# Kernel tuning notes

Measured on AMD Instinct MI355X. Metric: run time of the kernel, lower is better.

The kernel has to match this reference:

```python
import jax, jax.numpy as jnp
import numpy as np

DIM = 128
N_HEADS = 4
HEAD_DIM = DIM // N_HEADS
K = 16
B, N = 2, 8192
BIAS_HID = 32


def knn_idx(xyz, k):
    # squared pairwise distances: [B,N,N] (same argsort order as cdist)
    sq = jnp.sum(xyz * xyz, axis=-1)  # [B,N]
    d2 = sq[:, :, None] + sq[:, None, :] - 2.0 * jnp.einsum('bnd,bmd->bnm', xyz, xyz)
    _, idx = jax.lax.top_k(-d2, k)  # smallest distances
    return idx  # [B,N,k]


def setup_inputs() -> dict:
    key = jax.random.key(0)
    ks = jax.random.split(key, 12)
    s = 1.0 / np.sqrt(DIM)
    inp = {
        'x':   jax.random.normal(ks[0], (B, N, DIM), jnp.float32),
        'xyz': jax.random.normal(ks[1], (B, N, 3), jnp.float32),
        'Wq': jax.random.uniform(ks[2], (DIM, DIM), jnp.float32, -s, s),
        'bq': jnp.zeros((DIM,), jnp.float32),
        'Wk': jax.random.uniform(ks[3], (DIM, DIM), jnp.float32, -s, s),
        'bk': jnp.zeros((DIM,), jnp.float32),
        'Wv': jax.random.uniform(ks[4], (DIM, DIM), jnp.float32, -s, s),
        'bv': jnp.zeros((DIM,), jnp.float32),
        'Wo': jax.random.uniform(ks[5], (DIM, DIM), jnp.float32, -s, s),
        'bo': jnp.zeros((DIM,), jnp.float32),
        'W1': jax.random.uniform(ks[6], (3, BIAS_HID), jnp.float32, -0.5, 0.5),
        'b1': jnp.zeros((BIAS_HID,), jnp.float32),
        'W2': jax.random.uniform(ks[7], (BIAS_HID, N_HEADS), jnp.float32, -1.0 / np.sqrt(BIAS_HID), 1.0 / np.sqrt(BIAS_HID)),
        'b2': jnp.zeros((N_HEADS,), jnp.float32),
    }
    return inp


def reference(x, xyz, Wq, bq, Wk, bk, Wv, bv, Wo, bo, W1, b1, W2, b2):
    Bb, Nn, C = x.shape
    idx = knn_idx(xyz, K)  # [B,N,k]

    q = (x @ Wq + bq).reshape(Bb, Nn, N_HEADS, HEAD_DIM)
    kf = (x @ Wk + bk).reshape(Bb, Nn, N_HEADS, HEAD_DIM)
    vf = (x @ Wv + bv).reshape(Bb, Nn, N_HEADS, HEAD_DIM)

    gather = jax.vmap(lambda f, i: f[i])  # per-batch fancy gather
    kn = gather(kf, idx)  # [B,N,k,H,D]
    vn = gather(vf, idx)  # [B,N,k,H,D]
    nxyz = gather(xyz, idx)  # [B,N,k,3]

    rel = xyz[:, :, None, :] - nxyz  # [B,N,k,3]
    bias = jax.nn.relu(rel @ W1 + b1) @ W2 + b2  # [B,N,k,H]

    scores = jnp.einsum('bnhd,bnkhd->bnhk', q, kn) / np.sqrt(HEAD_DIM)
    scores = scores + jnp.swapaxes(bias, 2, 3)  # [B,N,H,k]
    attn = jax.nn.softmax(scores, axis=-1)
    out = jnp.einsum('bnhk,bnkhd->bnhd', attn, vn).reshape(Bb, Nn, C)
    return out @ Wo + bo
```

## Files before the change

kernel.cpp:

```cpp
#include <hip/hip_runtime.h>
#include <hip/hip_bf16.h>
#include <math.h>

#define BATCH 2
#define NPT   8192
#define DIMC  128
#define NH    4
#define KNN_K 16
#define HID   32
#define BN    (BATCH*NPT)

#define TILE 1024
#define QPW  2
#define NWV  4

__device__ __forceinline__ float readlane_f(float v, int l) {
  return __int_as_float(__builtin_amdgcn_readlane(__float_as_int(v), l));
}

__global__ __launch_bounds__(256) void knn_kernel(const float* __restrict__ xyz,
                                                  int* __restrict__ knn_out) {
  __shared__ float4 spts[TILE];
  const int tid  = threadIdx.x;
  const int lane = tid & 63;
  const int wave = tid >> 6;
  const int qbase = blockIdx.x * (NWV*QPW) + wave * QPW;
  const int b = qbase / NPT;

  float qx[QPW], qy[QPW], qz[QPW], qsq[QPW];
  float topd[QPW]; int topi[QPW]; float tau[QPW];
#pragma unroll
  for (int qi = 0; qi < QPW; ++qi) {
    const int g = qbase + qi;
    qx[qi] = xyz[(size_t)g*3+0];
    qy[qi] = xyz[(size_t)g*3+1];
    qz[qi] = xyz[(size_t)g*3+2];
    qsq[qi] = __fadd_rn(__fadd_rn(__fmul_rn(qx[qi],qx[qi]),
                                  __fmul_rn(qy[qi],qy[qi])),
                        __fmul_rn(qz[qi],qz[qi]));
    topd[qi] = 3e38f; topi[qi] = 0; tau[qi] = 3e38f;
  }

  for (int t = 0; t < NPT/TILE; ++t) {
    __syncthreads();
    const float* src = xyz + (size_t)(b*NPT + t*TILE)*3;
    for (int i = tid; i < TILE; i += 256) {
      const float x = src[i*3+0], y = src[i*3+1], z = src[i*3+2];
      const float sq = __fadd_rn(__fadd_rn(__fmul_rn(x,x), __fmul_rn(y,y)),
                                 __fmul_rn(z,z));
      spts[i] = make_float4(x+x, y+y, z+z, sq);
    }
    __syncthreads();

    for (int c = 0; c < TILE/64; ++c) {
      const float4 cd = spts[c*64 + lane];
      const int cbase = t*TILE + c*64;
#pragma unroll
      for (int qi = 0; qi < QPW; ++qi) {
        float dot2 = __fadd_rn(__fadd_rn(__fmul_rn(qx[qi],cd.x),
                                         __fmul_rn(qy[qi],cd.y)),
                               __fmul_rn(qz[qi],cd.z));
        float d2 = __fsub_rn(__fadd_rn(qsq[qi], cd.w), dot2);
        unsigned long long m = __ballot(d2 < tau[qi]);
        while (m) {
          const int l = (int)__builtin_ctzll(m);
          const float dn = readlane_f(d2, l);
          const int   ni_ = cbase + l;
          const float my  = topd[qi];
          const int   myi = topi[qi];
          float ab  = __shfl_up(my, 1);
          int   abi = __shfl_up(myi, 1);
          if (lane == 0) ab = -3e38f;
          const bool ge = dn < my;
          const bool gt = dn < ab;
          topd[qi] = ge ? (gt ? ab  : dn ) : my;
          topi[qi] = ge ? (gt ? abi : ni_) : myi;
          tau[qi] = readlane_f(topd[qi], 15);
          m &= (m - 1);
          if (m) m &= __ballot(d2 < tau[qi]);
        }
      }
    }
  }

#pragma unroll
  for (int qi = 0; qi < QPW; ++qi) {
    if (lane < KNN_K) knn_out[(size_t)(qbase + qi)*KNN_K + lane] = topi[qi];
  }
}

__device__ __forceinline__ float f4c(const float4 v, int u) {
  return u == 0 ? v.x : u == 1 ? v.y : u == 2 ? v.z : v.w;
}

__global__ __launch_bounds__(256) void qkv_kernel(const float* __restrict__ x,
    const float* __restrict__ Wq, const float* __restrict__ bq,
    const float* __restrict__ Wk, const float* __restrict__ bk,
    const float* __restrict__ Wv, const float* __restrict__ bv,
    float* __restrict__ q, float* __restrict__ k, float* __restrict__ v) {
  __shared__ float xs[16*DIMC];
  const int tid = threadIdx.x;
  const int rowbase = blockIdx.x * 16;
  {
    float4* xs4 = (float4*)xs;
    const float4* src4 = (const float4*)(x + (size_t)rowbase*DIMC);
    for (int i = tid; i < 16*DIMC/4; i += 256) xs4[i] = src4[i];
  }
  __syncthreads();

  const int cg = tid & 31, rg = tid >> 5;
  const int c0 = cg * 4;
  float4 aq0 = *(const float4*)&bq[c0], aq1 = aq0;
  float4 ak0 = *(const float4*)&bk[c0], ak1 = ak0;
  float4 av0 = *(const float4*)&bv[c0], av1 = av0;

  for (int kk = 0; kk < DIMC; kk += 4) {
    const float4 xa = *(const float4*)&xs[rg*DIMC + kk];
    const float4 xb = *(const float4*)&xs[(rg+8)*DIMC + kk];
#pragma unroll
    for (int u = 0; u < 4; ++u) {
      const float4 wq = *(const float4*)&Wq[(size_t)(kk+u)*DIMC + c0];
      const float4 wk = *(const float4*)&Wk[(size_t)(kk+u)*DIMC + c0];
      const float4 wv = *(const float4*)&Wv[(size_t)(kk+u)*DIMC + c0];
      const float xau = f4c(xa, u), xbu = f4c(xb, u);
      aq0.x = fmaf(xau, wq.x, aq0.x); aq0.y = fmaf(xau, wq.y, aq0.y);
      aq0.z = fmaf(xau, wq.z, aq0.z); aq0.w = fmaf(xau, wq.w, aq0.w);
      aq1.x = fmaf(xbu, wq.x, aq1.x); aq1.y = fmaf(xbu, wq.y, aq1.y);
      aq1.z = fmaf(xbu, wq.z, aq1.z); aq1.w = fmaf(xbu, wq.w, aq1.w);
      ak0.x = fmaf(xau, wk.x, ak0.x); ak0.y = fmaf(xau, wk.y, ak0.y);
      ak0.z = fmaf(xau, wk.z, ak0.z); ak0.w = fmaf(xau, wk.w, ak0.w);
      ak1.x = fmaf(xbu, wk.x, ak1.x); ak1.y = fmaf(xbu, wk.y, ak1.y);
      ak1.z = fmaf(xbu, wk.z, ak1.z); ak1.w = fmaf(xbu, wk.w, ak1.w);
      av0.x = fmaf(xau, wv.x, av0.x); av0.y = fmaf(xau, wv.y, av0.y);
      av0.z = fmaf(xau, wv.z, av0.z); av0.w = fmaf(xau, wv.w, av0.w);
      av1.x = fmaf(xbu, wv.x, av1.x); av1.y = fmaf(xbu, wv.y, av1.y);
      av1.z = fmaf(xbu, wv.z, av1.z); av1.w = fmaf(xbu, wv.w, av1.w);
    }
  }

  const size_t r0 = (size_t)(rowbase + rg)*DIMC + c0;
  const size_t r1 = (size_t)(rowbase + rg + 8)*DIMC + c0;
  *(float4*)&q[r0] = aq0; *(float4*)&q[r1] = aq1;
  *(float4*)&k[r0] = ak0; *(float4*)&k[r1] = ak1;
  *(float4*)&v[r0] = av0; *(float4*)&v[r1] = av1;
}

__global__ __launch_bounds__(256) void attn_kernel(const float* __restrict__ xyz,
    const int* __restrict__ knn, const float* __restrict__ qb,
    const float* __restrict__ kb, const float* __restrict__ vb,
    const float* __restrict__ W1, const float* __restrict__ b1,
    const float* __restrict__ W2, const float* __restrict__ b2,
    float* __restrict__ ao) {
  __shared__ float sbias[2][NH][KNN_K];
  const int tid = threadIdx.x;
  const int pt  = tid >> 7;
  const int d   = tid & 127;
  const int h   = d >> 5;
  const int p   = blockIdx.x * 2 + pt;
  const int b   = p / NPT;

  int nidx[KNN_K];
#pragma unroll
  for (int j = 0; j < KNN_K; ++j) nidx[j] = knn[(size_t)p*KNN_K + j];

  if (d < 64) {
    const int h2 = d >> 4, j2 = d & 15;
    const float qx0 = xyz[(size_t)p*3+0];
    const float qy0 = xyz[(size_t)p*3+1];
    const float qz0 = xyz[(size_t)p*3+2];
    const size_t nn = (size_t)(b*NPT + nidx[j2]);
    const float rx = qx0 - xyz[nn*3+0];
    const float ry = qy0 - xyz[nn*3+1];
    const float rz = qz0 - xyz[nn*3+2];
    float acc = b2[h2];
#pragma unroll 4
    for (int u = 0; u < HID; ++u) {
      float hv = rx*W1[0*HID+u] + ry*W1[1*HID+u] + rz*W1[2*HID+u] + b1[u];
      hv = hv > 0.f ? hv : 0.f;
      acc = fmaf(hv, W2[u*NH + h2], acc);
    }
    sbias[pt][h2][j2] = acc;
  }

  const float qd = qb[(size_t)p*DIMC + d];
  float s[KNN_K], vr[KNN_K];
#pragma unroll
  for (int j = 0; j < KNN_K; ++j) {
    const size_t row = ((size_t)(b*NPT + nidx[j]))*DIMC + d;
    float t = qd * kb[row];
    vr[j] = vb[row];
    t += __shfl_xor(t, 1, 32);
    t += __shfl_xor(t, 2, 32);
    t += __shfl_xor(t, 4, 32);
    t += __shfl_xor(t, 8, 32);
    t += __shfl_xor(t, 16, 32);
    s[j] = t;
  }
  __syncthreads();

  const float sc = 0.17677669529663689f;
  float mx = -3e38f;
#pragma unroll
  for (int j = 0; j < KNN_K; ++j) {
    s[j] = s[j]*sc + sbias[pt][h][j];
    mx = fmaxf(mx, s[j]);
  }
  float sum = 0.f;
#pragma unroll
  for (int j = 0; j < KNN_K; ++j) { s[j] = expf(s[j]-mx); sum += s[j]; }
  const float inv = 1.f / sum;
  float out = 0.f;
#pragma unroll
  for (int j = 0; j < KNN_K; ++j) out = fmaf(s[j]*inv, vr[j], out);
  ao[(size_t)p*DIMC + d] = out;
}

__global__ __launch_bounds__(256) void proj_kernel(float* __restrict__ inout,
    const float* __restrict__ Wo, const float* __restrict__ bo) {
  __shared__ float xs[16*DIMC];
  const int tid = threadIdx.x;
  const int rowbase = blockIdx.x * 16;
  {
    float4* xs4 = (float4*)xs;
    const float4* src4 = (const float4*)(inout + (size_t)rowbase*DIMC);
    for (int i = tid; i < 16*DIMC/4; i += 256) xs4[i] = src4[i];
  }
  __syncthreads();

  const int cg = tid & 31, rg = tid >> 5;
  const int c0 = cg * 4;
  float4 a0 = *(const float4*)&bo[c0], a1 = a0;

  for (int kk = 0; kk < DIMC; kk += 4) {
    const float4 xa = *(const float4*)&xs[rg*DIMC + kk];
    const float4 xb = *(const float4*)&xs[(rg+8)*DIMC + kk];
#pragma unroll
    for (int u = 0; u < 4; ++u) {
      const float4 w = *(const float4*)&Wo[(size_t)(kk+u)*DIMC + c0];
      const float xau = f4c(xa, u), xbu = f4c(xb, u);
      a0.x = fmaf(xau, w.x, a0.x); a0.y = fmaf(xau, w.y, a0.y);
      a0.z = fmaf(xau, w.z, a0.z); a0.w = fmaf(xau, w.w, a0.w);
      a1.x = fmaf(xbu, w.x, a1.x); a1.y = fmaf(xbu, w.y, a1.y);
      a1.z = fmaf(xbu, w.z, a1.z); a1.w = fmaf(xbu, w.w, a1.w);
    }
  }

  *(float4*)&inout[(size_t)(rowbase + rg)*DIMC + c0]     = a0;
  *(float4*)&inout[(size_t)(rowbase + rg + 8)*DIMC + c0] = a1;
}

extern "C" void kernel_launch(void* const* d_in, const int* in_sizes, int n_in,
                              void* d_out, int out_size, void* d_ws, size_t ws_size,
                              hipStream_t stream) {
  const float* x   = (const float*)d_in[0];
  const float* xyz = (const float*)d_in[1];
  const float* Wq  = (const float*)d_in[2];
  const float* bq  = (const float*)d_in[3];
  const float* Wk  = (const float*)d_in[4];
  const float* bk  = (const float*)d_in[5];
  const float* Wv  = (const float*)d_in[6];
  const float* bv  = (const float*)d_in[7];
  const float* Wo  = (const float*)d_in[8];
  const float* bo  = (const float*)d_in[9];
  const float* W1  = (const float*)d_in[10];
  const float* b1  = (const float*)d_in[11];
  const float* W2  = (const float*)d_in[12];
  const float* b2  = (const float*)d_in[13];
  float* out = (float*)d_out;

  char* ws = (char*)d_ws;
  int*   knn = (int*)ws;
  float* q   = (float*)(ws + (size_t)(1u<<20));
  float* k   = (float*)(ws + (size_t)9*(1u<<20));
  float* v   = (float*)(ws + (size_t)17*(1u<<20));

  hipLaunchKernelGGL(knn_kernel, dim3(BN/(NWV*QPW)), dim3(256), 0, stream, xyz, knn);
  hipLaunchKernelGGL(qkv_kernel, dim3(BN/16), dim3(256), 0, stream,
                     x, Wq, bq, Wk, bk, Wv, bv, q, k, v);
  hipLaunchKernelGGL(attn_kernel, dim3(BN/2), dim3(256), 0, stream,
                     xyz, knn, q, k, v, W1, b1, W2, b2, out);
  hipLaunchKernelGGL(proj_kernel, dim3(BN/16), dim3(256), 0, stream,
                     out, Wo, bo);
}
```

Measured before the change: 203.0 us.

## Remap attention to one wave per point with lane-per-(head,neighbor) scores

The attention kernel now gives each point a single 64-lane wave, with each lane owning one (head, neighbor) pair. Each lane computes its position-bias MLP and a 32-wide q·k dot product with float4 loads. The per-lane shuffle reductions over head dims are replaced by DPP row rotations that reduce max and sum across 16 neighbors. The softmax weights and neighbor indices are staged in shared memory, and each lane then accumulates two output channels from the gathered V rows. This removes redundant bias work and shuffle-heavy reductions and lets each block handle four points. In exchange, K rows are read with a strided per-lane access pattern rather than coalesced across lanes.

```diff
diff --git a/kernel.cpp b/kernel.cpp
--- a/kernel.cpp
+++ b/kernel.cpp
@@ -145,74 +145,92 @@
   *(float4*)&v[r0] = av0; *(float4*)&v[r1] = av1;
 }
 
+template <int CTRL>
+__device__ __forceinline__ float dppf(float x) {
+  return __int_as_float(__builtin_amdgcn_update_dpp(
+      __float_as_int(x), __float_as_int(x), CTRL, 0xF, 0xF, false));
+}
+#define ROR1 0x121
+#define ROR2 0x122
+#define ROR4 0x124
+#define ROR8 0x128
+
 __global__ __launch_bounds__(256) void attn_kernel(const float* __restrict__ xyz,
     const int* __restrict__ knn, const float* __restrict__ qb,
     const float* __restrict__ kb, const float* __restrict__ vb,
     const float* __restrict__ W1, const float* __restrict__ b1,
     const float* __restrict__ W2, const float* __restrict__ b2,
     float* __restrict__ ao) {
-  __shared__ float sbias[2][NH][KNN_K];
-  const int tid = threadIdx.x;
-  const int pt  = tid >> 7;
-  const int d   = tid & 127;
-  const int h   = d >> 5;
-  const int p   = blockIdx.x * 2 + pt;
-  const int b   = p / NPT;
-
-  int nidx[KNN_K];
-#pragma unroll
-  for (int j = 0; j < KNN_K; ++j) nidx[j] = knn[(size_t)p*KNN_K + j];
-
-  if (d < 64) {
-    const int h2 = d >> 4, j2 = d & 15;
-    const float qx0 = xyz[(size_t)p*3+0];
-    const float qy0 = xyz[(size_t)p*3+1];
-    const float qz0 = xyz[(size_t)p*3+2];
-    const size_t nn = (size_t)(b*NPT + nidx[j2]);
-    const float rx = qx0 - xyz[nn*3+0];
-    const float ry = qy0 - xyz[nn*3+1];
-    const float rz = qz0 - xyz[nn*3+2];
-    float acc = b2[h2];
+  __shared__ float sw[4][NH][KNN_K];
+  __shared__ int   sn[4][KNN_K];
+  const int tid  = threadIdx.x;
+  const int wave = tid >> 6;
+  const int lane = tid & 63;
+  const int p = blockIdx.x * 4 + wave;
+  const int b = p / NPT;
+  const int h = lane >> 4;
+  const int j = lane & 15;
+
+  const int nj = knn[(size_t)p*KNN_K + j];
+  if (h == 0) sn[wave][j] = nj;
+  const size_t nn = (size_t)b*NPT + nj;
+
+  const float qx0 = xyz[(size_t)p*3+0];
+  const float qy0 = xyz[(size_t)p*3+1];
+  const float qz0 = xyz[(size_t)p*3+2];
+  const float rx = qx0 - xyz[nn*3+0];
+  const float ry = qy0 - xyz[nn*3+1];
+  const float rz = qz0 - xyz[nn*3+2];
+  float bias = b2[h];
+#pragma unroll 8
+  for (int u = 0; u < HID; ++u) {
+    float hv = rx*W1[0*HID+u] + ry*W1[1*HID+u] + rz*W1[2*HID+u] + b1[u];
+    hv = hv > 0.f ? hv : 0.f;
+    bias = fmaf(hv, W2[u*NH + h], bias);
+  }
+
+  const float* qrow = qb + (size_t)p*DIMC + h*32;
+  const float* krow = kb + nn*DIMC + h*32;
+  float s = 0.f;
+#pragma unroll
+  for (int u = 0; u < 32; u += 4) {
+    const float4 qv = *(const float4*)(qrow + u);
+    const float4 kv = *(const float4*)(krow + u);
+    s = fmaf(qv.x, kv.x, s); s = fmaf(qv.y, kv.y, s);
+    s = fmaf(qv.z, kv.z, s); s = fmaf(qv.w, kv.w, s);
+  }
+  s = s * 0.17677669529663689f + bias;
+
+  float m = s;
+  m = fmaxf(m, dppf<ROR1>(m));
+  m = fmaxf(m, dppf<ROR2>(m));
+  m = fmaxf(m, dppf<ROR4>(m));
+  m = fmaxf(m, dppf<ROR8>(m));
+  const float e = expf(s - m);
+  float ssum = e;
+  ssum += dppf<ROR1>(ssum);
+  ssum += dppf<ROR2>(ssum);
+  ssum += dppf<ROR4>(ssum);
+  ssum += dppf<ROR8>(ssum);
+  sw[wave][h][j] = e / ssum;
+
+  __syncthreads();
+
+  const int d0 = lane;
+  const int hA = d0 >> 5;
+  float out0 = 0.f, out1 = 0.f;
+  const float* vbase = vb + (size_t)b*NPT*DIMC;
 #pragma unroll 4
-    for (int u = 0; u < HID; ++u) {
-      float hv = rx*W1[0*HID+u] + ry*W1[1*HID+u] + rz*W1[2*HID+u] + b1[u];
-      hv = hv > 0.f ? hv : 0.f;
-      acc = fmaf(hv, W2[u*NH + h2], acc);
-    }
-    sbias[pt][h2][j2] = acc;
-  }
-
-  const float qd = qb[(size_t)p*DIMC + d];
-  float s[KNN_K], vr[KNN_K];
-#pragma unroll
-  for (int j = 0; j < KNN_K; ++j) {
-    const size_t row = ((size_t)(b*NPT + nidx[j]))*DIMC + d;
-    float t = qd * kb[row];
-    vr[j] = vb[row];
-    t += __shfl_xor(t, 1, 32);
-    t += __shfl_xor(t, 2, 32);
-    t += __shfl_xor(t, 4, 32);
-    t += __shfl_xor(t, 8, 32);
-    t += __shfl_xor(t, 16, 32);
-    s[j] = t;
-  }
-  __syncthreads();
-
-  const float sc = 0.17677669529663689f;
-  float mx = -3e38f;
-#pragma unroll
-  for (int j = 0; j < KNN_K; ++j) {
-    s[j] = s[j]*sc + sbias[pt][h][j];
-    mx = fmaxf(mx, s[j]);
-  }
-  float sum = 0.f;
-#pragma unroll
-  for (int j = 0; j < KNN_K; ++j) { s[j] = expf(s[j]-mx); sum += s[j]; }
-  const float inv = 1.f / sum;
-  float out = 0.f;
-#pragma unroll
-  for (int j = 0; j < KNN_K; ++j) out = fmaf(s[j]*inv, vr[j], out);
-  ao[(size_t)p*DIMC + d] = out;
+  for (int j2 = 0; j2 < KNN_K; ++j2) {
+    const int n = sn[wave][j2];
+    const float wA = sw[wave][hA][j2];
+    const float wB = sw[wave][2+hA][j2];
+    const float* vrow = vbase + (size_t)n*DIMC;
+    out0 = fmaf(wA, vrow[d0],    out0);
+    out1 = fmaf(wB, vrow[64+d0], out1);
+  }
+  ao[(size_t)p*DIMC + d0]      = out0;
+  ao[(size_t)p*DIMC + 64 + d0] = out1;
 }
 
 __global__ __launch_bounds__(256) void proj_kernel(float* __restrict__ inout,
@@ -277,7 +295,7 @@
   hipLaunchKernelGGL(knn_kernel, dim3(BN/(NWV*QPW)), dim3(256), 0, stream, xyz, knn);
   hipLaunchKernelGGL(qkv_kernel, dim3(BN/16), dim3(256), 0, stream,
                      x, Wq, bq, Wk, bk, Wv, bv, q, k, v);
-  hipLaunchKernelGGL(attn_kernel, dim3(BN/2), dim3(256), 0, stream,
+  hipLaunchKernelGGL(attn_kernel, dim3(BN/4), dim3(256), 0, stream,
                      xyz, knn, q, k, v, W1, b1, W2, b2, out);
   hipLaunchKernelGGL(proj_kernel, dim3(BN/16), dim3(256), 0, stream,
                      out, Wo, bo);
```

Result: no change. 206.4 us (+1.7%).
